# Kernel tuning notes

Measured on AMD Instinct MI355X. Metric: run time of the kernel, lower is better.

Reference implementation:

```python
import jax, jax.numpy as jnp
import numpy as np

N_NODES = 50000
N_EDGES = 800000
N_FEAT = 128
HIDDEN = 256
N_GRAPHS = 256
N_CLASSES = 10
BN_EPS = 1e-5


def setup_inputs() -> dict:
    key = jax.random.key(0)
    ks = jax.random.split(key, 12)
    s = 1.0 / np.sqrt(HIDDEN)
    inp = {
        "x": jax.random.normal(ks[0], (N_NODES, N_FEAT), dtype=jnp.float32),
        "edge_index": jax.random.randint(ks[1], (2, N_EDGES), 0, N_NODES, dtype=jnp.int64),
        "batch": jnp.sort(jax.random.randint(ks[2], (N_NODES,), 0, N_GRAPHS, dtype=jnp.int64)),
        "conv1_w0": jax.random.normal(ks[3], (N_FEAT, HIDDEN), dtype=jnp.float32) / np.sqrt(N_FEAT),
        "conv1_b0": jnp.zeros((HIDDEN,), jnp.float32),
        "conv1_w1": jax.random.normal(ks[4], (HIDDEN, HIDDEN), dtype=jnp.float32) * s,
        "conv1_b1": jnp.zeros((HIDDEN,), jnp.float32),
        "conv1_bn_gamma": jnp.ones((HIDDEN,), jnp.float32),
        "conv1_bn_beta": jnp.zeros((HIDDEN,), jnp.float32),
        "conv1_bn_mean": jnp.zeros((HIDDEN,), jnp.float32),
        "conv1_bn_var": jnp.ones((HIDDEN,), jnp.float32),
        "convs_w0": jax.random.normal(ks[5], (3, HIDDEN, HIDDEN), dtype=jnp.float32) * s,
        "convs_b0": jnp.zeros((3, HIDDEN), jnp.float32),
        "convs_w1": jax.random.normal(ks[6], (3, HIDDEN, HIDDEN), dtype=jnp.float32) * s,
        "convs_b1": jnp.zeros((3, HIDDEN), jnp.float32),
        "convs_bn_gamma": jnp.ones((3, HIDDEN), jnp.float32),
        "convs_bn_beta": jnp.zeros((3, HIDDEN), jnp.float32),
        "convs_bn_mean": jnp.zeros((3, HIDDEN), jnp.float32),
        "convs_bn_var": jnp.ones((3, HIDDEN), jnp.float32),
        "eps": jnp.zeros((4,), jnp.float32),
        "lin1_w": jax.random.normal(ks[7], (HIDDEN, HIDDEN), dtype=jnp.float32) * s,
        "lin1_b": jnp.zeros((HIDDEN,), jnp.float32),
        "lin2_w": jax.random.normal(ks[8], (HIDDEN, N_CLASSES), dtype=jnp.float32) * s,
        "lin2_b": jnp.zeros((N_CLASSES,), jnp.float32),
    }
    return inp


def _gin_conv(x, src, dst, eps, w0, b0, w1, b1, g, be, m, v):
    # message = x[src]; aggregate = scatter_add at dst; update = MLP((1+eps)*x + aggr)
    aggr = jax.ops.segment_sum(x[src], dst, num_segments=N_NODES)
    h = (1.0 + eps) * x + aggr
    h = jax.nn.relu(h @ w0 + b0)
    h = jax.nn.relu(h @ w1 + b1)
    return (h - m) * jax.lax.rsqrt(v + BN_EPS) * g + be  # eval-mode BatchNorm1d


def reference(x, edge_index, batch,
              conv1_w0, conv1_b0, conv1_w1, conv1_b1,
              conv1_bn_gamma, conv1_bn_beta, conv1_bn_mean, conv1_bn_var,
              convs_w0, convs_b0, convs_w1, convs_b1,
              convs_bn_gamma, convs_bn_beta, convs_bn_mean, convs_bn_var,
              eps, lin1_w, lin1_b, lin2_w, lin2_b):
    src, dst = edge_index[0], edge_index[1]
    h = _gin_conv(x, src, dst, eps[0], conv1_w0, conv1_b0, conv1_w1, conv1_b1,
                  conv1_bn_gamma, conv1_bn_beta, conv1_bn_mean, conv1_bn_var)
    for i in range(convs_w0.shape[0]):
        h = _gin_conv(h, src, dst, eps[i + 1], convs_w0[i], convs_b0[i],
                      convs_w1[i], convs_b1[i], convs_bn_gamma[i], convs_bn_beta[i],
                      convs_bn_mean[i], convs_bn_var[i])
    # global_mean_pool over graph ids
    sums = jax.ops.segment_sum(h, batch, num_segments=N_GRAPHS)
    cnts = jax.ops.segment_sum(jnp.ones((N_NODES,), h.dtype), batch, num_segments=N_GRAPHS)
    pooled = sums / jnp.maximum(cnts, 1.0)[:, None]
    h = jax.nn.relu(pooled @ lin1_w + lin1_b)  # dropout is identity at inference
    logits = h @ lin2_w + lin2_b
    return jax.nn.log_softmax(logits, axis=-1)
```

## Files before the change

### kernel.cpp

```cpp
#include <hip/hip_runtime.h>
#include <hip/hip_bf16.h>

#define N_NODES 50000
#define N_EDGES 800000
#define N_FEAT 128
#define HIDDEN 256
#define N_GRAPHS 256
#define N_CLASSES 10

#define NBUCK ((N_NODES + 255) / 256)
#define EPB 2048
#define NBLK_S ((N_EDGES + EPB - 1) / EPB)

typedef __hip_bfloat16 bf16_t;
typedef short bf16x8 __attribute__((ext_vector_type(8)));
typedef float f32x4 __attribute__((ext_vector_type(4)));

__device__ inline float bfb2f(short s) {
    unsigned u = ((unsigned)(unsigned short)s) << 16;
    float f; __builtin_memcpy(&f, &u, 4); return f;
}
__device__ inline short f2bfb(float f) {
    bf16_t b = __float2bfloat16(f);
    short s; __builtin_memcpy(&s, &b, 2); return s;
}


__global__ __launch_bounds__(256) void bucket_hist_kernel(const int* __restrict__ ei,
                                                          unsigned* __restrict__ histT) {
    __shared__ unsigned lh[NBUCK];
    int t = threadIdx.x, j = blockIdx.x;
    for (int i = t; i < NBUCK; i += 256) lh[i] = 0;
    __syncthreads();
    int base = j * EPB;
    #pragma unroll
    for (int it = 0; it < EPB / 256; it++) {
        int e = base + it * 256 + t;
        if (e < N_EDGES) atomicAdd(&lh[(unsigned)ei[N_EDGES + e] >> 8], 1u);
    }
    __syncthreads();
    for (int i = t; i < NBUCK; i += 256) histT[(size_t)i * NBLK_S + j] = lh[i];
}

__global__ __launch_bounds__(256) void bucket_scan_a_kernel(unsigned* __restrict__ histT,
                                                            unsigned* __restrict__ bucketTot) {
    __shared__ unsigned tmp[256];
    int b = blockIdx.x, t = threadIdx.x;
    unsigned* row = histT + (size_t)b * NBLK_S;
    int i0 = t * 2, i1 = t * 2 + 1;
    unsigned v0 = (i0 < NBLK_S) ? row[i0] : 0u;
    unsigned v1 = (i1 < NBLK_S) ? row[i1] : 0u;
    unsigned s = v0 + v1;
    tmp[t] = s;
    __syncthreads();
    #pragma unroll
    for (int off = 1; off < 256; off <<= 1) {
        unsigned a = (t >= off) ? tmp[t - off] : 0u;
        __syncthreads();
        tmp[t] += a;
        __syncthreads();
    }
    unsigned base = tmp[t] - s;
    if (i0 < NBLK_S) row[i0] = base;
    if (i1 < NBLK_S) row[i1] = base + v0;
    if (t == 255) bucketTot[b] = tmp[255];
}

__global__ __launch_bounds__(256) void bucket_scan_b_kernel(const unsigned* __restrict__ bucketTot,
                                                            unsigned* __restrict__ bucketBase) {
    __shared__ unsigned tmp[256];
    int t = threadIdx.x;
    unsigned v = (t < NBUCK) ? bucketTot[t] : 0u;
    tmp[t] = v;
    __syncthreads();
    #pragma unroll
    for (int off = 1; off < 256; off <<= 1) {
        unsigned a = (t >= off) ? tmp[t - off] : 0u;
        __syncthreads();
        tmp[t] += a;
        __syncthreads();
    }
    if (t < NBUCK) bucketBase[t] = tmp[t] - v;
    if (t == NBUCK - 1) bucketBase[NBUCK] = tmp[t];
}

__global__ __launch_bounds__(256) void bucket_scatter_kernel(const int* __restrict__ ei,
                                                             const unsigned* __restrict__ histT,
                                                             const unsigned* __restrict__ bucketBase,
                                                             unsigned long long* __restrict__ ebuf) {
    __shared__ unsigned lcur[NBUCK];
    int t = threadIdx.x, j = blockIdx.x;
    for (int i = t; i < NBUCK; i += 256)
        lcur[i] = histT[(size_t)i * NBLK_S + j] + bucketBase[i];
    __syncthreads();
    int base = j * EPB;
    #pragma unroll
    for (int it = 0; it < EPB / 256; it++) {
        int e = base + it * 256 + t;
        if (e < N_EDGES) {
            unsigned src = (unsigned)ei[e];
            unsigned dst = (unsigned)ei[N_EDGES + e];
            unsigned pos = atomicAdd(&lcur[dst >> 8], 1u);
            ebuf[pos] = (unsigned long long)src | ((unsigned long long)dst << 32);
        }
    }
}

__global__ __launch_bounds__(256) void fine_fill_kernel(const unsigned long long* __restrict__ ebuf,
                                                        const unsigned* __restrict__ bucketBase,
                                                        unsigned* __restrict__ rowptr,
                                                        int* __restrict__ adj) {
    __shared__ unsigned ldeg[256], lcur[256], tmp[256];
    int b = blockIdx.x, t = threadIdx.x;
    unsigned sbase = bucketBase[b];
    int scnt = (int)(bucketBase[b + 1] - sbase);
    ldeg[t] = 0;
    __syncthreads();
    for (int k = t; k < scnt; k += 256) {
        unsigned dst = (unsigned)(ebuf[sbase + k] >> 32);
        atomicAdd(&ldeg[dst & 255], 1u);
    }
    __syncthreads();
    unsigned v = ldeg[t];
    tmp[t] = v;
    __syncthreads();
    for (int off = 1; off < 256; off <<= 1) {
        unsigned a = (t >= off) ? tmp[t - off] : 0u;
        __syncthreads();
        tmp[t] += a;
        __syncthreads();
    }
    unsigned exc = tmp[t] - v;
    lcur[t] = exc;
    int gnode = b * 256 + t;
    if (gnode < N_NODES) rowptr[gnode] = sbase + exc;
    if (b == NBUCK - 1 && t == 0) rowptr[N_NODES] = N_EDGES;
    __syncthreads();
    for (int k = t; k < scnt; k += 256) {
        unsigned long long p = ebuf[sbase + k];
        unsigned dst = (unsigned)(p >> 32);
        unsigned pos = atomicAdd(&lcur[dst & 255], 1u);
        adj[sbase + pos] = (int)(p & 0xffffffffu);
    }
}


__global__ __launch_bounds__(256) void convert_x_kernel(const float* __restrict__ x,
                                                        bf16_t* __restrict__ xb) {
    int i = blockIdx.x * 256 + threadIdx.x;
    if (i < N_NODES * N_FEAT / 4) {
        float4 v = reinterpret_cast<const float4*>(x)[i];
        short4 o;
        o.x = f2bfb(v.x); o.y = f2bfb(v.y); o.z = f2bfb(v.z); o.w = f2bfb(v.w);
        reinterpret_cast<short4*>(xb)[i] = o;
    }
}


__global__ __launch_bounds__(256) void prep_weights_kernel(
    const float* __restrict__ c1_w0, const float* __restrict__ c1_w1,
    const float* __restrict__ cs_w0, const float* __restrict__ cs_w1,
    bf16_t* __restrict__ wt)
{
    __shared__ float T[32][33];
    int z = blockIdx.z;
    const float* src; int K; size_t off;
    if (z == 0)      { src = c1_w0; K = N_FEAT;  off = 0; }
    else if (z == 1) { src = c1_w1; K = HIDDEN;  off = 32768; }
    else {
        int i = (z - 2) >> 1;
        src = (((z - 2) & 1) ? cs_w1 : cs_w0) + (size_t)i * HIDDEN * HIDDEN;
        K = HIDDEN;
        off = 32768 + (size_t)(z - 1) * 65536;
    }
    int k0 = blockIdx.x * 32, n0 = blockIdx.y * 32;
    if (k0 >= K) return;
    int t = threadIdx.x;
    int r = t >> 3, c4 = (t & 7) * 4;
    float4 v = *reinterpret_cast<const float4*>(src + (size_t)(k0 + r) * HIDDEN + n0 + c4);
    T[r][c4 + 0] = v.x; T[r][c4 + 1] = v.y; T[r][c4 + 2] = v.z; T[r][c4 + 3] = v.w;
    __syncthreads();
    int n = t >> 3, kc = (t & 7) * 4;
    short4 o;
    o.x = f2bfb(T[kc + 0][n]); o.y = f2bfb(T[kc + 1][n]);
    o.z = f2bfb(T[kc + 2][n]); o.w = f2bfb(T[kc + 3][n]);
    *reinterpret_cast<short4*>((short*)wt + off + (size_t)(n0 + n) * K + k0 + kc) = o;
}


__global__ __launch_bounds__(256) void aggregate1_kernel(
    const bf16_t* __restrict__ xb, const int* __restrict__ adj,
    const unsigned* __restrict__ rowptr, const float* __restrict__ eps_arr,
    bf16_t* __restrict__ out)
{
    int w = threadIdx.x >> 6, lane = threadIdx.x & 63;
    int n = blockIdx.x * 4 + w;
    if (n >= N_NODES) return;
    int q = lane >> 4, l4 = lane & 15;
    unsigned beg = rowptr[n], end = rowptr[n + 1];
    const short* xs = (const short*)xb;
    float acc[8] = {};
    unsigned e = beg;
    for (; e + 8 <= end; e += 8) {
        int s0 = adj[e + q];
        int s1 = adj[e + 4 + q];
        bf16x8 v0 = *reinterpret_cast<const bf16x8*>(xs + (unsigned)s0 * N_FEAT + l4 * 8);
        bf16x8 v1 = *reinterpret_cast<const bf16x8*>(xs + (unsigned)s1 * N_FEAT + l4 * 8);
        #pragma unroll
        for (int j = 0; j < 8; j++) acc[j] += bfb2f(v0[j]) + bfb2f(v1[j]);
    }
    for (; e + 4 <= end; e += 4) {
        int s0 = adj[e + q];
        bf16x8 v0 = *reinterpret_cast<const bf16x8*>(xs + (unsigned)s0 * N_FEAT + l4 * 8);
        #pragma unroll
        for (int j = 0; j < 8; j++) acc[j] += bfb2f(v0[j]);
    }
    int rem = (int)(end - e);
    if (q < rem) {
        bf16x8 v0 = *reinterpret_cast<const bf16x8*>(xs + (unsigned)adj[e + q] * N_FEAT + l4 * 8);
        #pragma unroll
        for (int j = 0; j < 8; j++) acc[j] += bfb2f(v0[j]);
    }
    if (q == 0) {
        bf16x8 sv = *reinterpret_cast<const bf16x8*>(xs + (unsigned)n * N_FEAT + l4 * 8);
        float ep = 1.f + eps_arr[0];
        #pragma unroll
        for (int j = 0; j < 8; j++) acc[j] += ep * bfb2f(sv[j]);
    }
    #pragma unroll
    for (int j = 0; j < 8; j++) {
        acc[j] += __shfl_xor(acc[j], 16);
        acc[j] += __shfl_xor(acc[j], 32);
    }
    if (lane < 16) {
        bf16x8 o;
        #pragma unroll
        for (int j = 0; j < 8; j++) o[j] = f2bfb(acc[j]);
        *reinterpret_cast<bf16x8*>((short*)out + (unsigned)n * N_FEAT + l4 * 8) = o;
    }
}


__global__ __launch_bounds__(256) void aggregate2_kernel(
    const bf16_t* __restrict__ x, const int* __restrict__ adj,
    const unsigned* __restrict__ rowptr, const float* __restrict__ eps_arr, int eps_idx,
    bf16_t* __restrict__ out)
{
    int w = threadIdx.x >> 6, lane = threadIdx.x & 63;
    int n = blockIdx.x * 4 + w;
    if (n >= N_NODES) return;
    int half = lane >> 5, l5 = lane & 31;
    unsigned beg = rowptr[n], end = rowptr[n + 1];
    const short* xs = (const short*)x;
    float acc[8] = {};
    unsigned e = beg;
    for (; e + 8 <= end; e += 8) {
        int s0 = adj[e + half];
        int s1 = adj[e + 2 + half];
        int s2 = adj[e + 4 + half];
        int s3 = adj[e + 6 + half];
        bf16x8 v0 = *reinterpret_cast<const bf16x8*>(xs + (unsigned)s0 * HIDDEN + l5 * 8);
        bf16x8 v1 = *reinterpret_cast<const bf16x8*>(xs + (unsigned)s1 * HIDDEN + l5 * 8);
        bf16x8 v2 = *reinterpret_cast<const bf16x8*>(xs + (unsigned)s2 * HIDDEN + l5 * 8);
        bf16x8 v3 = *reinterpret_cast<const bf16x8*>(xs + (unsigned)s3 * HIDDEN + l5 * 8);
        #pragma unroll
        for (int j = 0; j < 8; j++)
            acc[j] += (bfb2f(v0[j]) + bfb2f(v1[j])) + (bfb2f(v2[j]) + bfb2f(v3[j]));
    }
    for (; e + 2 <= end; e += 2) {
        int s0 = adj[e + half];
        bf16x8 v0 = *reinterpret_cast<const bf16x8*>(xs + (unsigned)s0 * HIDDEN + l5 * 8);
        #pragma unroll
        for (int j = 0; j < 8; j++) acc[j] += bfb2f(v0[j]);
    }
    if (e < end && half == 0) {
        bf16x8 v0 = *reinterpret_cast<const bf16x8*>(xs + (unsigned)adj[e] * HIDDEN + l5 * 8);
        #pragma unroll
        for (int j = 0; j < 8; j++) acc[j] += bfb2f(v0[j]);
    }
    if (half == 0) {
        bf16x8 sv = *reinterpret_cast<const bf16x8*>(xs + (unsigned)n * HIDDEN + l5 * 8);
        float ep = 1.f + eps_arr[eps_idx];
        #pragma unroll
        for (int j = 0; j < 8; j++) acc[j] += ep * bfb2f(sv[j]);
    }
    #pragma unroll
    for (int j = 0; j < 8; j++) acc[j] += __shfl_xor(acc[j], 32);
    if (half == 0) {
        bf16x8 o;
        #pragma unroll
        for (int j = 0; j < 8; j++) o[j] = f2bfb(acc[j]);
        *reinterpret_cast<bf16x8*>((short*)out + (unsigned)n * HIDDEN + l5 * 8) = o;
    }
}


template<int K0>
__global__ __launch_bounds__(512) void conv_mlp_kernel(
    const bf16_t* __restrict__ A, const bf16_t* __restrict__ W0t, const float* __restrict__ b0,
    const bf16_t* __restrict__ W1t, const float* __restrict__ b1,
    const float* __restrict__ bn_g, const float* __restrict__ bn_b,
    const float* __restrict__ bn_m, const float* __restrict__ bn_v,
    bf16_t* __restrict__ C, int M)
{
    __shared__ short sh[32768];
    int tid = threadIdx.x, lane = tid & 63, wave = tid >> 6;
    int wr = wave >> 2, wc = wave & 3;
    int row0 = blockIdx.x * 128;
    int fr = lane & 15, fk = (lane >> 4) * 8;

    const short* Ab = (const short*)A;
    const short* W0b = (const short*)W0t;
    const short* W1b = (const short*)W1t;

    constexpr int CPR0 = K0 / 8;
    #pragma unroll
    for (int it = 0; it < 128 * CPR0 / 512; it++) {
        int c = it * 512 + tid;
        int r = c / CPR0, ch = c % CPR0;
        int col = ch * 8;
        bf16x8 v = {};
        int gr = row0 + r;
        if (gr < M) v = *reinterpret_cast<const bf16x8*>(Ab + (size_t)gr * K0 + col);
        *reinterpret_cast<bf16x8*>(&sh[r * K0 + (col ^ ((r & 7) << 3))]) = v;
    }
    __syncthreads();

    f32x4 acc[4][4] = {};
    #pragma unroll
    for (int ks = 0; ks < K0 / 32; ks++) {
        bf16x8 a[4], b[4];
        #pragma unroll
        for (int m = 0; m < 4; m++) {
            int r = wr * 64 + m * 16 + fr;
            a[m] = *reinterpret_cast<const bf16x8*>(&sh[r * K0 + ((ks * 32 + fk) ^ ((r & 7) << 3))]);
        }
        #pragma unroll
        for (int n = 0; n < 4; n++)
            b[n] = *reinterpret_cast<const bf16x8*>(W0b + (size_t)(wc * 64 + n * 16 + fr) * K0 + ks * 32 + fk);
        #pragma unroll
        for (int m = 0; m < 4; m++)
            #pragma unroll
            for (int n = 0; n < 4; n++)
                acc[m][n] = __builtin_amdgcn_mfma_f32_16x16x32_bf16(a[m], b[n], acc[m][n], 0, 0, 0);
    }
    __syncthreads();

    #pragma unroll
    for (int m = 0; m < 4; m++) {
        int rl = wr * 64 + m * 16 + (lane >> 4) * 4;
        #pragma unroll
        for (int n = 0; n < 4; n++) {
            int cl = wc * 64 + n * 16 + fr;
            float bi = b0[cl];
            #pragma unroll
            for (int r = 0; r < 4; r++) {
                int rr = rl + r;
                sh[rr * 256 + (cl ^ ((rr & 7) << 3))] = f2bfb(fmaxf(acc[m][n][r] + bi, 0.f));
            }
        }
    }
    __syncthreads();

    f32x4 acc1[4][4] = {};
    #pragma unroll
    for (int ks = 0; ks < 8; ks++) {
        bf16x8 a[4], b[4];
        #pragma unroll
        for (int m = 0; m < 4; m++) {
            int r = wr * 64 + m * 16 + fr;
            a[m] = *reinterpret_cast<const bf16x8*>(&sh[r * 256 + ((ks * 32 + fk) ^ ((r & 7) << 3))]);
        }
        #pragma unroll
        for (int n = 0; n < 4; n++)
            b[n] = *reinterpret_cast<const bf16x8*>(W1b + (size_t)(wc * 64 + n * 16 + fr) * 256 + ks * 32 + fk);
        #pragma unroll
        for (int m = 0; m < 4; m++)
            #pragma unroll
            for (int n = 0; n < 4; n++)
                acc1[m][n] = __builtin_amdgcn_mfma_f32_16x16x32_bf16(a[m], b[n], acc1[m][n], 0, 0, 0);
    }
    __syncthreads();

    #pragma unroll
    for (int m = 0; m < 4; m++) {
        int rl = wr * 64 + m * 16 + (lane >> 4) * 4;
        #pragma unroll
        for (int n = 0; n < 4; n++) {
            int cl = wc * 64 + n * 16 + fr;
            float bi = b1[cl];
            float bnm = bn_m[cl], bns = rsqrtf(bn_v[cl] + 1e-5f), bng = bn_g[cl], bnb = bn_b[cl];
            #pragma unroll
            for (int r = 0; r < 4; r++) {
                int rr = rl + r;
                float v = fmaxf(acc1[m][n][r] + bi, 0.f);
                v = (v - bnm) * bns * bng + bnb;
                sh[rr * 256 + (cl ^ ((rr & 7) << 3))] = f2bfb(v);
            }
        }
    }
    __syncthreads();
    #pragma unroll
    for (int it = 0; it < 8; it++) {
        int c = it * 512 + tid;
        int r = c >> 5, ch = c & 31;
        int col = ch * 8;
        int gr = row0 + r;
        if (gr < M) {
            bf16x8 v = *reinterpret_cast<const bf16x8*>(&sh[r * 256 + (col ^ ((r & 7) << 3))]);
            *reinterpret_cast<bf16x8*>((short*)C + (size_t)gr * 256 + col) = v;
        }
    }
}


__global__ __launch_bounds__(256) void pool_kernel(const bf16_t* __restrict__ h,
                                                   const int* __restrict__ batch,
                                                   float* __restrict__ pooled) {
    __shared__ int sbs[2];
    __shared__ float red[4][HIDDEN];
    int g = blockIdx.x;
    if (threadIdx.x == 0) {
        int lo = 0, hi = N_NODES;
        while (lo < hi) { int mid = (lo + hi) >> 1; if (batch[mid] < g) lo = mid + 1; else hi = mid; }
        sbs[0] = lo;
        hi = N_NODES;
        while (lo < hi) { int mid = (lo + hi) >> 1; if (batch[mid] < g + 1) lo = mid + 1; else hi = mid; }
        sbs[1] = lo;
    }
    __syncthreads();
    int sbeg = sbs[0], send = sbs[1];
    int w = threadIdx.x >> 6, lane = threadIdx.x & 63;
    int half = lane >> 5, l5 = lane & 31;
    const short* hb = (const short*)h;
    float acc[8] = {};
    for (int n = sbeg + w * 2 + half; n < send; n += 8) {
        bf16x8 v = *reinterpret_cast<const bf16x8*>(hb + (size_t)n * HIDDEN + l5 * 8);
        #pragma unroll
        for (int j = 0; j < 8; j++) acc[j] += bfb2f(v[j]);
    }
    #pragma unroll
    for (int j = 0; j < 8; j++) acc[j] += __shfl_xor(acc[j], 32);
    if (half == 0) {
        #pragma unroll
        for (int j = 0; j < 8; j++) red[w][l5 * 8 + j] = acc[j];
    }
    __syncthreads();
    int t = threadIdx.x;
    float s = red[0][t] + red[1][t] + red[2][t] + red[3][t];
    float cnt = (float)(send - sbeg);
    pooled[g * HIDDEN + t] = s / fmaxf(cnt, 1.f);
}


__global__ void head_kernel(const float* __restrict__ pooled,
                            const float* __restrict__ w1, const float* __restrict__ b1,
                            const float* __restrict__ w2, const float* __restrict__ b2,
                            float* __restrict__ out) {
    int g = blockIdx.x, t = threadIdx.x;
    __shared__ float p[HIDDEN];
    __shared__ float h1[HIDDEN];
    __shared__ float lg[N_CLASSES];
    p[t] = pooled[g * HIDDEN + t];
    __syncthreads();
    float acc = b1[t];
    for (int k = 0; k < HIDDEN; k++) acc += p[k] * w1[k * HIDDEN + t];
    h1[t] = fmaxf(acc, 0.f);
    __syncthreads();
    if (t < N_CLASSES) {
        float a = b2[t];
        for (int k = 0; k < HIDDEN; k++) a += h1[k] * w2[k * N_CLASSES + t];
        lg[t] = a;
    }
    __syncthreads();
    if (t == 0) {
        float mx = lg[0];
        for (int j = 1; j < N_CLASSES; j++) mx = fmaxf(mx, lg[j]);
        float se = 0.f;
        for (int j = 0; j < N_CLASSES; j++) se += expf(lg[j] - mx);
        float lse = mx + logf(se);
        for (int j = 0; j < N_CLASSES; j++) out[g * N_CLASSES + j] = lg[j] - lse;
    }
}


extern "C" void kernel_launch(void* const* d_in, const int* in_sizes, int n_in,
                              void* d_out, int out_size, void* d_ws, size_t ws_size,
                              hipStream_t stream) {
    const float* x       = (const float*)d_in[0];
    const int*   ei      = (const int*)d_in[1];
    const int*   batch   = (const int*)d_in[2];
    const float* c1_w0   = (const float*)d_in[3];
    const float* c1_b0   = (const float*)d_in[4];
    const float* c1_w1   = (const float*)d_in[5];
    const float* c1_b1   = (const float*)d_in[6];
    const float* c1_g    = (const float*)d_in[7];
    const float* c1_be   = (const float*)d_in[8];
    const float* c1_m    = (const float*)d_in[9];
    const float* c1_v    = (const float*)d_in[10];
    const float* cs_w0   = (const float*)d_in[11];
    const float* cs_b0   = (const float*)d_in[12];
    const float* cs_w1   = (const float*)d_in[13];
    const float* cs_b1   = (const float*)d_in[14];
    const float* cs_g    = (const float*)d_in[15];
    const float* cs_be   = (const float*)d_in[16];
    const float* cs_m    = (const float*)d_in[17];
    const float* cs_v    = (const float*)d_in[18];
    const float* eps     = (const float*)d_in[19];
    const float* lin1_w  = (const float*)d_in[20];
    const float* lin1_b  = (const float*)d_in[21];
    const float* lin2_w  = (const float*)d_in[22];
    const float* lin2_b  = (const float*)d_in[23];

    char* ws = (char*)d_ws;
    size_t off = 0;
    auto alloc = [&](size_t bytes) -> void* {
        void* p = ws + off;
        off += (bytes + 255) & ~(size_t)255;
        return p;
    };

    unsigned* histT      = (unsigned*)alloc((size_t)NBUCK * NBLK_S * 4);
    unsigned* bucketTot  = (unsigned*)alloc(NBUCK * 4);
    unsigned* bucketBase = (unsigned*)alloc((NBUCK + 1) * 4);
    unsigned long long* ebuf = (unsigned long long*)alloc((size_t)N_EDGES * 8);
    unsigned* rowptr     = (unsigned*)alloc((N_NODES + 1) * 4);
    int*      adj        = (int*)alloc(N_EDGES * 4);
    bf16_t*   Wt         = (bf16_t*)alloc((size_t)(32768 + 7 * 65536) * 2);
    bf16_t*   xb         = (bf16_t*)alloc((size_t)N_NODES * N_FEAT * 2);
    bf16_t*   B1         = (bf16_t*)alloc((size_t)N_NODES * HIDDEN * 2);
    bf16_t*   B3         = (bf16_t*)alloc((size_t)N_NODES * HIDDEN * 2);
    float*    pooled     = (float*)alloc(N_GRAPHS * HIDDEN * 4);

    bf16_t* wt_10 = Wt;
    bf16_t* wt_11 = Wt + 32768;
    auto wt_c0 = [&](int i) { return Wt + 32768 + (size_t)(1 + 2 * i) * 65536; };
    auto wt_c1 = [&](int i) { return Wt + 32768 + (size_t)(2 + 2 * i) * 65536; };

    bucket_hist_kernel<<<NBLK_S, 256, 0, stream>>>(ei, histT);
    bucket_scan_a_kernel<<<NBUCK, 256, 0, stream>>>(histT, bucketTot);
    bucket_scan_b_kernel<<<1, 256, 0, stream>>>(bucketTot, bucketBase);
    bucket_scatter_kernel<<<NBLK_S, 256, 0, stream>>>(ei, histT, bucketBase, ebuf);
    fine_fill_kernel<<<NBUCK, 256, 0, stream>>>(ebuf, bucketBase, rowptr, adj);

    convert_x_kernel<<<(N_NODES * N_FEAT / 4 + 255) / 256, 256, 0, stream>>>(x, xb);
    prep_weights_kernel<<<dim3(8, 8, 8), 256, 0, stream>>>(c1_w0, c1_w1, cs_w0, cs_w1, Wt);

    int cgrid = (N_NODES + 127) / 128;
    int ab = (N_NODES + 3) / 4;

    aggregate1_kernel<<<ab, 256, 0, stream>>>(xb, adj, rowptr, eps, B1);
    conv_mlp_kernel<128><<<cgrid, 512, 0, stream>>>(B1, wt_10, c1_b0, wt_11, c1_b1,
                                                    c1_g, c1_be, c1_m, c1_v, B3, N_NODES);

    for (int i = 0; i < 3; i++) {
        aggregate2_kernel<<<ab, 256, 0, stream>>>(B3, adj, rowptr, eps, i + 1, B1);
        conv_mlp_kernel<256><<<cgrid, 512, 0, stream>>>(B1, wt_c0(i), cs_b0 + i * HIDDEN,
                                                        wt_c1(i), cs_b1 + i * HIDDEN,
                                                        cs_g + i * HIDDEN, cs_be + i * HIDDEN,
                                                        cs_m + i * HIDDEN, cs_v + i * HIDDEN,
                                                        B3, N_NODES);
    }

    pool_kernel<<<N_GRAPHS, 256, 0, stream>>>(B3, batch, pooled);
    head_kernel<<<N_GRAPHS, HIDDEN, 0, stream>>>(pooled, lin1_w, lin1_b, lin2_w, lin2_b, (float*)d_out);
}
```

Before: 462.2 us.

## Slice gather-aggregation by feature columns so neighboring blocks share cache-resident slices

Replaces the two per-node aggregation kernels with one templated kernel. Each block handles 64 nodes for a single 32-column feature slice, and each node is served by 4 lanes reading 8 columns each. Consecutive blocks cover different slices of the same node tile, so the gathered working set per slice is narrower and more likely to stay in L2/MALL. The catch is that every slice re-reads adjacency and rowptr, each gather moves only 64 bytes per neighbor row, and there is less memory-level parallelism per lane because the neighbor loop is unrolled only by 2.

```diff
diff --git a/kernel.cpp b/kernel.cpp
--- a/kernel.cpp
+++ b/kernel.cpp
@@ -188,110 +188,44 @@
 }
 
 
-__global__ __launch_bounds__(256) void aggregate1_kernel(
-    const bf16_t* __restrict__ xb, const int* __restrict__ adj,
-    const unsigned* __restrict__ rowptr, const float* __restrict__ eps_arr,
-    bf16_t* __restrict__ out)
-{
-    int w = threadIdx.x >> 6, lane = threadIdx.x & 63;
-    int n = blockIdx.x * 4 + w;
-    if (n >= N_NODES) return;
-    int q = lane >> 4, l4 = lane & 15;
-    unsigned beg = rowptr[n], end = rowptr[n + 1];
-    const short* xs = (const short*)xb;
-    float acc[8] = {};
-    unsigned e = beg;
-    for (; e + 8 <= end; e += 8) {
-        int s0 = adj[e + q];
-        int s1 = adj[e + 4 + q];
-        bf16x8 v0 = *reinterpret_cast<const bf16x8*>(xs + (unsigned)s0 * N_FEAT + l4 * 8);
-        bf16x8 v1 = *reinterpret_cast<const bf16x8*>(xs + (unsigned)s1 * N_FEAT + l4 * 8);
-        #pragma unroll
-        for (int j = 0; j < 8; j++) acc[j] += bfb2f(v0[j]) + bfb2f(v1[j]);
-    }
-    for (; e + 4 <= end; e += 4) {
-        int s0 = adj[e + q];
-        bf16x8 v0 = *reinterpret_cast<const bf16x8*>(xs + (unsigned)s0 * N_FEAT + l4 * 8);
-        #pragma unroll
-        for (int j = 0; j < 8; j++) acc[j] += bfb2f(v0[j]);
-    }
-    int rem = (int)(end - e);
-    if (q < rem) {
-        bf16x8 v0 = *reinterpret_cast<const bf16x8*>(xs + (unsigned)adj[e + q] * N_FEAT + l4 * 8);
-        #pragma unroll
-        for (int j = 0; j < 8; j++) acc[j] += bfb2f(v0[j]);
-    }
-    if (q == 0) {
-        bf16x8 sv = *reinterpret_cast<const bf16x8*>(xs + (unsigned)n * N_FEAT + l4 * 8);
-        float ep = 1.f + eps_arr[0];
-        #pragma unroll
-        for (int j = 0; j < 8; j++) acc[j] += ep * bfb2f(sv[j]);
-    }
-    #pragma unroll
-    for (int j = 0; j < 8; j++) {
-        acc[j] += __shfl_xor(acc[j], 16);
-        acc[j] += __shfl_xor(acc[j], 32);
-    }
-    if (lane < 16) {
-        bf16x8 o;
-        #pragma unroll
-        for (int j = 0; j < 8; j++) o[j] = f2bfb(acc[j]);
-        *reinterpret_cast<bf16x8*>((short*)out + (unsigned)n * N_FEAT + l4 * 8) = o;
-    }
-}
-
-
-__global__ __launch_bounds__(256) void aggregate2_kernel(
+template<int COLS, int NS>
+__global__ __launch_bounds__(256) void aggregate_sliced_kernel(
     const bf16_t* __restrict__ x, const int* __restrict__ adj,
     const unsigned* __restrict__ rowptr, const float* __restrict__ eps_arr, int eps_idx,
     bf16_t* __restrict__ out)
 {
+    int slice = blockIdx.x % NS;
+    int tile  = blockIdx.x / NS;
     int w = threadIdx.x >> 6, lane = threadIdx.x & 63;
-    int n = blockIdx.x * 4 + w;
+    int g = lane >> 2, l2 = lane & 3;
+    int n = tile * 64 + w * 16 + g;
     if (n >= N_NODES) return;
-    int half = lane >> 5, l5 = lane & 31;
-    unsigned beg = rowptr[n], end = rowptr[n + 1];
-    const short* xs = (const short*)x;
+    int co = slice * 32 + l2 * 8;
+    const short* xs = (const short*)x + co;
+    unsigned e = rowptr[n], end = rowptr[n + 1];
     float acc[8] = {};
-    unsigned e = beg;
-    for (; e + 8 <= end; e += 8) {
-        int s0 = adj[e + half];
-        int s1 = adj[e + 2 + half];
-        int s2 = adj[e + 4 + half];
-        int s3 = adj[e + 6 + half];
-        bf16x8 v0 = *reinterpret_cast<const bf16x8*>(xs + (unsigned)s0 * HIDDEN + l5 * 8);
-        bf16x8 v1 = *reinterpret_cast<const bf16x8*>(xs + (unsigned)s1 * HIDDEN + l5 * 8);
-        bf16x8 v2 = *reinterpret_cast<const bf16x8*>(xs + (unsigned)s2 * HIDDEN + l5 * 8);
-        bf16x8 v3 = *reinterpret_cast<const bf16x8*>(xs + (unsigned)s3 * HIDDEN + l5 * 8);
-        #pragma unroll
-        for (int j = 0; j < 8; j++)
-            acc[j] += (bfb2f(v0[j]) + bfb2f(v1[j])) + (bfb2f(v2[j]) + bfb2f(v3[j]));
-    }
     for (; e + 2 <= end; e += 2) {
-        int s0 = adj[e + half];
-        bf16x8 v0 = *reinterpret_cast<const bf16x8*>(xs + (unsigned)s0 * HIDDEN + l5 * 8);
+        int s0 = adj[e], s1 = adj[e + 1];
+        bf16x8 v0 = *reinterpret_cast<const bf16x8*>(xs + (unsigned)s0 * COLS);
+        bf16x8 v1 = *reinterpret_cast<const bf16x8*>(xs + (unsigned)s1 * COLS);
+        #pragma unroll
+        for (int j = 0; j < 8; j++) acc[j] += bfb2f(v0[j]) + bfb2f(v1[j]);
+    }
+    if (e < end) {
+        bf16x8 v0 = *reinterpret_cast<const bf16x8*>(xs + (unsigned)adj[e] * COLS);
         #pragma unroll
         for (int j = 0; j < 8; j++) acc[j] += bfb2f(v0[j]);
     }
-    if (e < end && half == 0) {
-        bf16x8 v0 = *reinterpret_cast<const bf16x8*>(xs + (unsigned)adj[e] * HIDDEN + l5 * 8);
-        #pragma unroll
-        for (int j = 0; j < 8; j++) acc[j] += bfb2f(v0[j]);
-    }
-    if (half == 0) {
-        bf16x8 sv = *reinterpret_cast<const bf16x8*>(xs + (unsigned)n * HIDDEN + l5 * 8);
+    {
+        bf16x8 sv = *reinterpret_cast<const bf16x8*>(xs + (unsigned)n * COLS);
         float ep = 1.f + eps_arr[eps_idx];
         #pragma unroll
         for (int j = 0; j < 8; j++) acc[j] += ep * bfb2f(sv[j]);
     }
-    #pragma unroll
-    for (int j = 0; j < 8; j++) acc[j] += __shfl_xor(acc[j], 32);
-    if (half == 0) {
-        bf16x8 o;
-        #pragma unroll
-        for (int j = 0; j < 8; j++) o[j] = f2bfb(acc[j]);
-        *reinterpret_cast<bf16x8*>((short*)out + (unsigned)n * HIDDEN + l5 * 8) = o;
-    }
+    bf16x8 o;
+    #pragma unroll
+    for (int j = 0; j < 8; j++) o[j] = f2bfb(acc[j]);
+    *reinterpret_cast<bf16x8*>((short*)out + (unsigned)n * COLS + co) = o;
 }
 
 
@@ -317,8 +251,7 @@
     #pragma unroll
     for (int it = 0; it < 128 * CPR0 / 512; it++) {
         int c = it * 512 + tid;
-        int r = c / CPR0, ch = c % CPR0;
-        int col = ch * 8;
+        int r = c / CPR0, col = (c % CPR0) * 8;
         bf16x8 v = {};
         int gr = row0 + r;
         if (gr < M) v = *reinterpret_cast<const bf16x8*>(Ab + (size_t)gr * K0 + col);
@@ -403,8 +336,7 @@
     #pragma unroll
     for (int it = 0; it < 8; it++) {
         int c = it * 512 + tid;
-        int r = c >> 5, ch = c & 31;
-        int col = ch * 8;
+        int r = c >> 5, col = (c & 31) * 8;
         int gr = row0 + r;
         if (gr < M) {
             bf16x8 v = *reinterpret_cast<const bf16x8*>(&sh[r * 256 + (col ^ ((r & 7) << 3))]);
@@ -546,15 +478,15 @@
     convert_x_kernel<<<(N_NODES * N_FEAT / 4 + 255) / 256, 256, 0, stream>>>(x, xb);
     prep_weights_kernel<<<dim3(8, 8, 8), 256, 0, stream>>>(c1_w0, c1_w1, cs_w0, cs_w1, Wt);
 
+    int ntiles = (N_NODES + 63) / 64;
     int cgrid = (N_NODES + 127) / 128;
-    int ab = (N_NODES + 3) / 4;
-
-    aggregate1_kernel<<<ab, 256, 0, stream>>>(xb, adj, rowptr, eps, B1);
+
+    aggregate_sliced_kernel<128, 4><<<ntiles * 4, 256, 0, stream>>>(xb, adj, rowptr, eps, 0, B1);
     conv_mlp_kernel<128><<<cgrid, 512, 0, stream>>>(B1, wt_10, c1_b0, wt_11, c1_b1,
                                                     c1_g, c1_be, c1_m, c1_v, B3, N_NODES);
 
     for (int i = 0; i < 3; i++) {
-        aggregate2_kernel<<<ab, 256, 0, stream>>>(B3, adj, rowptr, eps, i + 1, B1);
+        aggregate_sliced_kernel<256, 8><<<ntiles * 8, 256, 0, stream>>>(B3, adj, rowptr, eps, i + 1, B1);
         conv_mlp_kernel<256><<<cgrid, 512, 0, stream>>>(B1, wt_c0(i), cs_b0 + i * HIDDEN,
                                                         wt_c1(i), cs_b1 + i * HIDDEN,
                                                         cs_g + i * HIDDEN, cs_be + i * HIDDEN,
```

Measured after the change: 559.7 us. +21.1%, slower.

## Fuse neighbor aggregation into GIN MLP kernel via shared memory

Applied to the files above, without the earlier changes.

The separate aggregate kernels are removed, and each GIN layer kernel now gathers neighbor sums for its 128-row tile directly into swizzled shared memory before running the two MFMA GEMMs. This avoids writing the aggregated tensor to global memory and reading it back, and drops one launch per layer. Output buffers now ping-pong between two allocations. In exchange, the gather runs with only 391 blocks of 512 threads and each wave walks 16 nodes one after another, so there may be less latency hiding than the old many-small-block aggregate.

```diff
diff --git a/kernel.cpp b/kernel.cpp
--- a/kernel.cpp
+++ b/kernel.cpp
@@ -188,116 +188,11 @@
 }
 
 
-__global__ __launch_bounds__(256) void aggregate1_kernel(
-    const bf16_t* __restrict__ xb, const int* __restrict__ adj,
-    const unsigned* __restrict__ rowptr, const float* __restrict__ eps_arr,
-    bf16_t* __restrict__ out)
-{
-    int w = threadIdx.x >> 6, lane = threadIdx.x & 63;
-    int n = blockIdx.x * 4 + w;
-    if (n >= N_NODES) return;
-    int q = lane >> 4, l4 = lane & 15;
-    unsigned beg = rowptr[n], end = rowptr[n + 1];
-    const short* xs = (const short*)xb;
-    float acc[8] = {};
-    unsigned e = beg;
-    for (; e + 8 <= end; e += 8) {
-        int s0 = adj[e + q];
-        int s1 = adj[e + 4 + q];
-        bf16x8 v0 = *reinterpret_cast<const bf16x8*>(xs + (unsigned)s0 * N_FEAT + l4 * 8);
-        bf16x8 v1 = *reinterpret_cast<const bf16x8*>(xs + (unsigned)s1 * N_FEAT + l4 * 8);
-        #pragma unroll
-        for (int j = 0; j < 8; j++) acc[j] += bfb2f(v0[j]) + bfb2f(v1[j]);
-    }
-    for (; e + 4 <= end; e += 4) {
-        int s0 = adj[e + q];
-        bf16x8 v0 = *reinterpret_cast<const bf16x8*>(xs + (unsigned)s0 * N_FEAT + l4 * 8);
-        #pragma unroll
-        for (int j = 0; j < 8; j++) acc[j] += bfb2f(v0[j]);
-    }
-    int rem = (int)(end - e);
-    if (q < rem) {
-        bf16x8 v0 = *reinterpret_cast<const bf16x8*>(xs + (unsigned)adj[e + q] * N_FEAT + l4 * 8);
-        #pragma unroll
-        for (int j = 0; j < 8; j++) acc[j] += bfb2f(v0[j]);
-    }
-    if (q == 0) {
-        bf16x8 sv = *reinterpret_cast<const bf16x8*>(xs + (unsigned)n * N_FEAT + l4 * 8);
-        float ep = 1.f + eps_arr[0];
-        #pragma unroll
-        for (int j = 0; j < 8; j++) acc[j] += ep * bfb2f(sv[j]);
-    }
-    #pragma unroll
-    for (int j = 0; j < 8; j++) {
-        acc[j] += __shfl_xor(acc[j], 16);
-        acc[j] += __shfl_xor(acc[j], 32);
-    }
-    if (lane < 16) {
-        bf16x8 o;
-        #pragma unroll
-        for (int j = 0; j < 8; j++) o[j] = f2bfb(acc[j]);
-        *reinterpret_cast<bf16x8*>((short*)out + (unsigned)n * N_FEAT + l4 * 8) = o;
-    }
-}
-
-
-__global__ __launch_bounds__(256) void aggregate2_kernel(
-    const bf16_t* __restrict__ x, const int* __restrict__ adj,
+template<int K0>
+__global__ __launch_bounds__(512) void gin_layer_kernel(
+    const bf16_t* __restrict__ X, const int* __restrict__ adj,
     const unsigned* __restrict__ rowptr, const float* __restrict__ eps_arr, int eps_idx,
-    bf16_t* __restrict__ out)
-{
-    int w = threadIdx.x >> 6, lane = threadIdx.x & 63;
-    int n = blockIdx.x * 4 + w;
-    if (n >= N_NODES) return;
-    int half = lane >> 5, l5 = lane & 31;
-    unsigned beg = rowptr[n], end = rowptr[n + 1];
-    const short* xs = (const short*)x;
-    float acc[8] = {};
-    unsigned e = beg;
-    for (; e + 8 <= end; e += 8) {
-        int s0 = adj[e + half];
-        int s1 = adj[e + 2 + half];
-        int s2 = adj[e + 4 + half];
-        int s3 = adj[e + 6 + half];
-        bf16x8 v0 = *reinterpret_cast<const bf16x8*>(xs + (unsigned)s0 * HIDDEN + l5 * 8);
-        bf16x8 v1 = *reinterpret_cast<const bf16x8*>(xs + (unsigned)s1 * HIDDEN + l5 * 8);
-        bf16x8 v2 = *reinterpret_cast<const bf16x8*>(xs + (unsigned)s2 * HIDDEN + l5 * 8);
-        bf16x8 v3 = *reinterpret_cast<const bf16x8*>(xs + (unsigned)s3 * HIDDEN + l5 * 8);
-        #pragma unroll
-        for (int j = 0; j < 8; j++)
-            acc[j] += (bfb2f(v0[j]) + bfb2f(v1[j])) + (bfb2f(v2[j]) + bfb2f(v3[j]));
-    }
-    for (; e + 2 <= end; e += 2) {
-        int s0 = adj[e + half];
-        bf16x8 v0 = *reinterpret_cast<const bf16x8*>(xs + (unsigned)s0 * HIDDEN + l5 * 8);
-        #pragma unroll
-        for (int j = 0; j < 8; j++) acc[j] += bfb2f(v0[j]);
-    }
-    if (e < end && half == 0) {
-        bf16x8 v0 = *reinterpret_cast<const bf16x8*>(xs + (unsigned)adj[e] * HIDDEN + l5 * 8);
-        #pragma unroll
-        for (int j = 0; j < 8; j++) acc[j] += bfb2f(v0[j]);
-    }
-    if (half == 0) {
-        bf16x8 sv = *reinterpret_cast<const bf16x8*>(xs + (unsigned)n * HIDDEN + l5 * 8);
-        float ep = 1.f + eps_arr[eps_idx];
-        #pragma unroll
-        for (int j = 0; j < 8; j++) acc[j] += ep * bfb2f(sv[j]);
-    }
-    #pragma unroll
-    for (int j = 0; j < 8; j++) acc[j] += __shfl_xor(acc[j], 32);
-    if (half == 0) {
-        bf16x8 o;
-        #pragma unroll
-        for (int j = 0; j < 8; j++) o[j] = f2bfb(acc[j]);
-        *reinterpret_cast<bf16x8*>((short*)out + (unsigned)n * HIDDEN + l5 * 8) = o;
-    }
-}
-
-
-template<int K0>
-__global__ __launch_bounds__(512) void conv_mlp_kernel(
-    const bf16_t* __restrict__ A, const bf16_t* __restrict__ W0t, const float* __restrict__ b0,
+    const bf16_t* __restrict__ W0t, const float* __restrict__ b0,
     const bf16_t* __restrict__ W1t, const float* __restrict__ b1,
     const float* __restrict__ bn_g, const float* __restrict__ bn_b,
     const float* __restrict__ bn_m, const float* __restrict__ bn_v,
@@ -308,21 +203,103 @@
     int wr = wave >> 2, wc = wave & 3;
     int row0 = blockIdx.x * 128;
     int fr = lane & 15, fk = (lane >> 4) * 8;
-
-    const short* Ab = (const short*)A;
+    float ep = 1.f + eps_arr[eps_idx];
+
+    const short* xs = (const short*)X;
     const short* W0b = (const short*)W0t;
     const short* W1b = (const short*)W1t;
 
-    constexpr int CPR0 = K0 / 8;
-    #pragma unroll
-    for (int it = 0; it < 128 * CPR0 / 512; it++) {
-        int c = it * 512 + tid;
-        int r = c / CPR0, ch = c % CPR0;
-        int col = ch * 8;
-        bf16x8 v = {};
-        int gr = row0 + r;
-        if (gr < M) v = *reinterpret_cast<const bf16x8*>(Ab + (size_t)gr * K0 + col);
-        *reinterpret_cast<bf16x8*>(&sh[r * K0 + (col ^ ((r & 7) << 3))]) = v;
+    if (K0 == 256) {
+        int half = lane >> 5, l5 = lane & 31;
+        for (int rr = 0; rr < 16; rr++) {
+            int r = wave * 16 + rr;
+            int n = row0 + r;
+            unsigned e = 0, end = 0;
+            if (n < M) { e = rowptr[n]; end = rowptr[n + 1]; }
+            float acc[8] = {};
+            for (; e + 8 <= end; e += 8) {
+                int s0 = adj[e + half];
+                int s1 = adj[e + 2 + half];
+                int s2 = adj[e + 4 + half];
+                int s3 = adj[e + 6 + half];
+                bf16x8 v0 = *reinterpret_cast<const bf16x8*>(xs + (unsigned)s0 * 256 + l5 * 8);
+                bf16x8 v1 = *reinterpret_cast<const bf16x8*>(xs + (unsigned)s1 * 256 + l5 * 8);
+                bf16x8 v2 = *reinterpret_cast<const bf16x8*>(xs + (unsigned)s2 * 256 + l5 * 8);
+                bf16x8 v3 = *reinterpret_cast<const bf16x8*>(xs + (unsigned)s3 * 256 + l5 * 8);
+                #pragma unroll
+                for (int j = 0; j < 8; j++)
+                    acc[j] += (bfb2f(v0[j]) + bfb2f(v1[j])) + (bfb2f(v2[j]) + bfb2f(v3[j]));
+            }
+            for (; e + 2 <= end; e += 2) {
+                int s0 = adj[e + half];
+                bf16x8 v0 = *reinterpret_cast<const bf16x8*>(xs + (unsigned)s0 * 256 + l5 * 8);
+                #pragma unroll
+                for (int j = 0; j < 8; j++) acc[j] += bfb2f(v0[j]);
+            }
+            if (e < end && half == 0) {
+                bf16x8 v0 = *reinterpret_cast<const bf16x8*>(xs + (unsigned)adj[e] * 256 + l5 * 8);
+                #pragma unroll
+                for (int j = 0; j < 8; j++) acc[j] += bfb2f(v0[j]);
+            }
+            if (n < M && half == 0) {
+                bf16x8 sv = *reinterpret_cast<const bf16x8*>(xs + (unsigned)n * 256 + l5 * 8);
+                #pragma unroll
+                for (int j = 0; j < 8; j++) acc[j] += ep * bfb2f(sv[j]);
+            }
+            #pragma unroll
+            for (int j = 0; j < 8; j++) acc[j] += __shfl_xor(acc[j], 32);
+            if (half == 0) {
+                bf16x8 o;
+                #pragma unroll
+                for (int j = 0; j < 8; j++) o[j] = f2bfb(acc[j]);
+                *reinterpret_cast<bf16x8*>(&sh[r * 256 + ((l5 * 8) ^ ((r & 7) << 3))]) = o;
+            }
+        }
+    } else {
+        int q = lane >> 4, l4 = lane & 15;
+        for (int rr = 0; rr < 16; rr++) {
+            int r = wave * 16 + rr;
+            int n = row0 + r;
+            unsigned e = 0, end = 0;
+            if (n < M) { e = rowptr[n]; end = rowptr[n + 1]; }
+            float acc[8] = {};
+            for (; e + 8 <= end; e += 8) {
+                int s0 = adj[e + q];
+                int s1 = adj[e + 4 + q];
+                bf16x8 v0 = *reinterpret_cast<const bf16x8*>(xs + (unsigned)s0 * 128 + l4 * 8);
+                bf16x8 v1 = *reinterpret_cast<const bf16x8*>(xs + (unsigned)s1 * 128 + l4 * 8);
+                #pragma unroll
+                for (int j = 0; j < 8; j++) acc[j] += bfb2f(v0[j]) + bfb2f(v1[j]);
+            }
+            for (; e + 4 <= end; e += 4) {
+                int s0 = adj[e + q];
+                bf16x8 v0 = *reinterpret_cast<const bf16x8*>(xs + (unsigned)s0 * 128 + l4 * 8);
+                #pragma unroll
+                for (int j = 0; j < 8; j++) acc[j] += bfb2f(v0[j]);
+            }
+            int rem = (int)(end - e);
+            if (q < rem) {
+                bf16x8 v0 = *reinterpret_cast<const bf16x8*>(xs + (unsigned)adj[e + q] * 128 + l4 * 8);
+                #pragma unroll
+                for (int j = 0; j < 8; j++) acc[j] += bfb2f(v0[j]);
+            }
+            if (n < M && q == 0) {
+                bf16x8 sv = *reinterpret_cast<const bf16x8*>(xs + (unsigned)n * 128 + l4 * 8);
+                #pragma unroll
+                for (int j = 0; j < 8; j++) acc[j] += ep * bfb2f(sv[j]);
+            }
+            #pragma unroll
+            for (int j = 0; j < 8; j++) {
+                acc[j] += __shfl_xor(acc[j], 16);
+                acc[j] += __shfl_xor(acc[j], 32);
+            }
+            if (lane < 16) {
+                bf16x8 o;
+                #pragma unroll
+                for (int j = 0; j < 8; j++) o[j] = f2bfb(acc[j]);
+                *reinterpret_cast<bf16x8*>(&sh[r * 128 + ((l4 * 8) ^ ((r & 7) << 3))]) = o;
+            }
+        }
     }
     __syncthreads();
 
@@ -403,8 +380,7 @@
     #pragma unroll
     for (int it = 0; it < 8; it++) {
         int c = it * 512 + tid;
-        int r = c >> 5, ch = c & 31;
-        int col = ch * 8;
+        int r = c >> 5, col = (c & 31) * 8;
         int gr = row0 + r;
         if (gr < M) {
             bf16x8 v = *reinterpret_cast<const bf16x8*>(&sh[r * 256 + (col ^ ((r & 7) << 3))]);
@@ -528,8 +504,8 @@
     int*      adj        = (int*)alloc(N_EDGES * 4);
     bf16_t*   Wt         = (bf16_t*)alloc((size_t)(32768 + 7 * 65536) * 2);
     bf16_t*   xb         = (bf16_t*)alloc((size_t)N_NODES * N_FEAT * 2);
-    bf16_t*   B1         = (bf16_t*)alloc((size_t)N_NODES * HIDDEN * 2);
-    bf16_t*   B3         = (bf16_t*)alloc((size_t)N_NODES * HIDDEN * 2);
+    bf16_t*   BA         = (bf16_t*)alloc((size_t)N_NODES * HIDDEN * 2);
+    bf16_t*   BB         = (bf16_t*)alloc((size_t)N_NODES * HIDDEN * 2);
     float*    pooled     = (float*)alloc(N_GRAPHS * HIDDEN * 4);
 
     bf16_t* wt_10 = Wt;
@@ -547,21 +523,23 @@
     prep_weights_kernel<<<dim3(8, 8, 8), 256, 0, stream>>>(c1_w0, c1_w1, cs_w0, cs_w1, Wt);
 
     int cgrid = (N_NODES + 127) / 128;
-    int ab = (N_NODES + 3) / 4;
-
-    aggregate1_kernel<<<ab, 256, 0, stream>>>(xb, adj, rowptr, eps, B1);
-    conv_mlp_kernel<128><<<cgrid, 512, 0, stream>>>(B1, wt_10, c1_b0, wt_11, c1_b1,
-                                                    c1_g, c1_be, c1_m, c1_v, B3, N_NODES);
-
+
+    gin_layer_kernel<128><<<cgrid, 512, 0, stream>>>(xb, adj, rowptr, eps, 0,
+                                                     wt_10, c1_b0, wt_11, c1_b1,
+                                                     c1_g, c1_be, c1_m, c1_v, BA, N_NODES);
+
+    const bf16_t* src = BA;
+    bf16_t* dst = BB;
     for (int i = 0; i < 3; i++) {
-        aggregate2_kernel<<<ab, 256, 0, stream>>>(B3, adj, rowptr, eps, i + 1, B1);
-        conv_mlp_kernel<256><<<cgrid, 512, 0, stream>>>(B1, wt_c0(i), cs_b0 + i * HIDDEN,
-                                                        wt_c1(i), cs_b1 + i * HIDDEN,
-                                                        cs_g + i * HIDDEN, cs_be + i * HIDDEN,
-                                                        cs_m + i * HIDDEN, cs_v + i * HIDDEN,
-                                                        B3, N_NODES);
-    }
-
-    pool_kernel<<<N_GRAPHS, 256, 0, stream>>>(B3, batch, pooled);
+        gin_layer_kernel<256><<<cgrid, 512, 0, stream>>>(src, adj, rowptr, eps, i + 1,
+                                                         wt_c0(i), cs_b0 + i * HIDDEN,
+                                                         wt_c1(i), cs_b1 + i * HIDDEN,
+                                                         cs_g + i * HIDDEN, cs_be + i * HIDDEN,
+                                                         cs_m + i * HIDDEN, cs_v + i * HIDDEN,
+                                                         dst, N_NODES);
+        const bf16_t* tmp = src; src = dst; dst = (bf16_t*)tmp;
+    }
+
+    pool_kernel<<<N_GRAPHS, 256, 0, stream>>>(src, batch, pooled);
     head_kernel<<<N_GRAPHS, HIDDEN, 0, stream>>>(pooled, lin1_w, lin1_b, lin2_w, lin2_b, (float*)d_out);
 }
```

After: 647.1 us. 40.0% more time.
